# Optimization experiments

Measured on AMD Instinct MI355X. Metric: run time of the kernel, lower is better.

Reference implementation:

```python
import jax, jax.numpy as jnp
import numpy as np


def _conv(x, w, b, stride, pad):
    y = jax.lax.conv_general_dilated(
        x, w, (stride, stride), [(pad, pad), (pad, pad)],
        dimension_numbers=('NCHW', 'OIHW', 'NCHW'))
    return y + b[None, :, None, None]


def _maxpool(x):
    # kernel 3, stride 2, padding 1 (torch MaxPool2d semantics)
    return jax.lax.reduce_window(
        x, -jnp.inf, jax.lax.max,
        (1, 1, 3, 3), (1, 1, 2, 2), [(0, 0), (0, 0), (1, 1), (1, 1)])


def _squash(s, eps=1e-8):
    n2 = jnp.sum(s * s, axis=-1, keepdims=True)
    return s * (n2 / (1.0 + n2)) / jnp.sqrt(n2 + eps)


def setup_inputs() -> dict:
    key = jax.random.key(0)
    ks = jax.random.split(key, 17)
    s = 0.05
    inp = {
        'x': jax.random.normal(ks[0], (128, 3, 32, 32), jnp.float32),
        'cw1': jax.random.normal(ks[1], (96, 3, 3, 3), jnp.float32) * s,
        'cb1': jnp.zeros((96,), jnp.float32),
        'cw2': jax.random.normal(ks[2], (256, 96, 3, 3), jnp.float32) * s,
        'cb2': jnp.zeros((256,), jnp.float32),
        'cw3': jax.random.normal(ks[3], (384, 256, 3, 3), jnp.float32) * s,
        'cb3': jnp.zeros((384,), jnp.float32),
        'pw': jax.random.normal(ks[4], (256, 384, 3, 3), jnp.float32) * s,  # 32 caps * 8 dim
        'pb': jnp.zeros((256,), jnp.float32),
        'Wcaps': jax.random.normal(ks[5], (100, 1152, 16, 8), jnp.float32) * s,
        'fw1': jax.random.normal(ks[6], (1600, 4096), jnp.float32) * s,
        'fb1': jnp.zeros((4096,), jnp.float32),
        'fw2': jax.random.normal(ks[7], (4096, 4096), jnp.float32) * s,
        'fb2': jnp.zeros((4096,), jnp.float32),
        'fw3': jax.random.normal(ks[8], (4096, 100), jnp.float32) * s,
        'fb3': jnp.zeros((100,), jnp.float32),
    }
    return inp


def reference(x, cw1, cb1, cw2, cb2, cw3, cb3, pw, pb, Wcaps,
              fw1, fb1, fw2, fb2, fw3, fb3):
    ROUTINGS = 3
    # AlexNet-style conv backbone
    h = jax.nn.relu(_conv(x, cw1, cb1, 1, 1))   # [B,96,32,32]
    h = _maxpool(h)                              # [B,96,16,16]
    h = jax.nn.relu(_conv(h, cw2, cb2, 1, 1))   # [B,256,16,16]
    h = _maxpool(h)                              # [B,256,8,8]
    h = jax.nn.relu(_conv(h, cw3, cb3, 1, 1))   # [B,384,8,8]
    # PrimaryCaps: conv 384 -> 32*8, k3 s1 p0 -> [B,256,6,6]
    p = _conv(h, pw, pb, 1, 0)
    u = _squash(p.reshape(p.shape[0], -1, 8))   # [B,1152,8]
    # DenseCapsule: x_hat[b,o,i,d] = sum_e W[o,i,d,e] * u[b,i,e]
    x_hat = jnp.einsum('oide,bie->boid', Wcaps, u)  # [B,100,1152,16]
    x_hat_d = jax.lax.stop_gradient(x_hat)
    b = jnp.zeros(x_hat.shape[:3], x_hat.dtype)     # [B,100,1152]
    v = None
    for r in range(ROUTINGS):
        c = jax.nn.softmax(b, axis=1)               # couple over out caps
        if r == ROUTINGS - 1:
            v = _squash(jnp.einsum('boi,boid->bod', c, x_hat))
        else:
            v = _squash(jnp.einsum('boi,boid->bod', c, x_hat_d))
            b = b + jnp.einsum('boid,bod->boi', x_hat_d, v)
    # Flatten + FC head (dropout is identity at eval)
    f = v.reshape(v.shape[0], -1)                   # [B,1600]
    f = jax.nn.relu(f @ fw1 + fb1)
    f = jax.nn.relu(f @ fw2 + fb2)
    return f @ fw3 + fb3                            # [B,100]
```

## Files before the change

### kernel.cpp

```cpp
#include <hip/hip_runtime.h>
#include <cstddef>


typedef __attribute__((ext_vector_type(8))) short bf8_t;
typedef __attribute__((ext_vector_type(4))) float f4_t;

__device__ inline void cvt_hilo8(const float* f, unsigned* h, unsigned* l)
{
  #pragma unroll
  for (int j = 0; j < 4; ++j) {
    unsigned u0 = __float_as_uint(f[2 * j]);
    unsigned u1 = __float_as_uint(f[2 * j + 1]);
    h[j] = (u0 >> 16) | (u1 & 0xFFFF0000u);
    float r0 = f[2 * j]     - __uint_as_float(u0 & 0xFFFF0000u);
    float r1 = f[2 * j + 1] - __uint_as_float(u1 & 0xFFFF0000u);
    l[j] = (__float_as_uint(r0) >> 16) | (__float_as_uint(r1) & 0xFFFF0000u);
  }
}

__device__ inline void split1(float f, unsigned short& h, unsigned short& l)
{
  unsigned u = __float_as_uint(f);
  h = (unsigned short)(u >> 16);
  float r = f - __uint_as_float(u & 0xFFFF0000u);
  l = (unsigned short)(__float_as_uint(r) >> 16);
}

__device__ inline float bf2f(unsigned short h, unsigned short l)
{
  return __uint_as_float((unsigned)h << 16) + __uint_as_float((unsigned)l << 16);
}

__device__ inline int xcd_swz(int bid, int nwg)
{
  int xcd = bid & 7, pos = bid >> 3;
  int q = nwg >> 3, r = nwg & 7;
  return (xcd < r ? xcd * (q + 1) : r * (q + 1) + (xcd - r) * q) + pos;
}

__global__ __launch_bounds__(256) void wsplit_k(
    const float* __restrict__ w, unsigned short* __restrict__ oh,
    unsigned short* __restrict__ ol, int CO, int CI)
{
  int idx = blockIdx.x * 256 + threadIdx.x;
  int ci = idx % CI;
  int t2 = idx / CI;
  int r = t2 % 9, co = t2 / 9;
  float f = w[((size_t)co * CI + ci) * 9 + r];
  unsigned short h, l;
  split1(f, h, l);
  oh[idx] = h; ol[idx] = l;
}

__global__ __launch_bounds__(256) void conv1_k(
    const float* __restrict__ x, const float* __restrict__ wt,
    const float* __restrict__ bias, unsigned short* __restrict__ oh,
    unsigned short* __restrict__ ol)
{
  int idx = blockIdx.x * 256 + threadIdx.x;
  int w = idx & 31, h = (idx >> 5) & 31, b = idx >> 10;
  int co0 = blockIdx.y * 24;

  float xv[27];
  const float* xb = x + (size_t)b * 3072;
  #pragma unroll
  for (int ci = 0; ci < 3; ++ci)
    #pragma unroll
    for (int dh = 0; dh < 3; ++dh) {
      int ih = h + dh - 1;
      #pragma unroll
      for (int dw = 0; dw < 3; ++dw) {
        int iw = w + dw - 1;
        bool ok = ((unsigned)ih < 32u) & ((unsigned)iw < 32u);
        xv[ci * 9 + dh * 3 + dw] = ok ? xb[(ci << 10) + (ih << 5) + iw] : 0.f;
      }
    }

  size_t obase = ((size_t)b * 1024 + (h << 5) + w) * 96 + co0;
  const float* wp = wt + (size_t)co0 * 27;
  #pragma unroll 2
  for (int cp = 0; cp < 12; ++cp) {
    float a0 = bias[co0 + 2 * cp], a1 = bias[co0 + 2 * cp + 1];
    #pragma unroll
    for (int k = 0; k < 27; ++k) {
      a0 += xv[k] * wp[(2 * cp) * 27 + k];
      a1 += xv[k] * wp[(2 * cp + 1) * 27 + k];
    }
    a0 = fmaxf(a0, 0.f); a1 = fmaxf(a1, 0.f);
    unsigned short h0, l0, h1, l1;
    split1(a0, h0, l0); split1(a1, h1, l1);
    *(unsigned*)(oh + obase + 2 * cp) = (unsigned)h0 | ((unsigned)h1 << 16);
    *(unsigned*)(ol + obase + 2 * cp) = (unsigned)l0 | ((unsigned)l1 << 16);
  }
}

template <int C, int H>
__global__ __launch_bounds__(256) void maxpool_bf(
    const unsigned short* __restrict__ inh, const unsigned short* __restrict__ inl,
    unsigned short* __restrict__ outh, unsigned short* __restrict__ outl)
{
  constexpr int Ho = H >> 1;
  int idx = blockIdx.x * 256 + threadIdx.x;
  int c = idx % C;
  int q = idx / C;
  int wo = q % Ho;
  int q2 = q / Ho;
  int ho = q2 % Ho, b = q2 / Ho;
  float best = -3.4e38f;
  unsigned short bh = 0, bl = 0;
  #pragma unroll
  for (int dh = 0; dh < 3; ++dh) {
    int ih = 2 * ho - 1 + dh;
    if ((unsigned)ih >= (unsigned)H) continue;
    #pragma unroll
    for (int dw = 0; dw < 3; ++dw) {
      int iw = 2 * wo - 1 + dw;
      if ((unsigned)iw >= (unsigned)H) continue;
      size_t off = ((size_t)(b * H + ih) * H + iw) * C + c;
      unsigned short uh = inh[off], ul = inl[off];
      float f = bf2f(uh, ul);
      if (f > best) { best = f; bh = uh; bl = ul; }
    }
  }
  outh[idx] = bh; outl[idx] = bl;
}

__global__ __launch_bounds__(256) void bias_split_k(
    const float* __restrict__ in, const float* __restrict__ bias,
    unsigned short* __restrict__ oh, unsigned short* __restrict__ ol,
    int C, int total2, int nz, size_t plane)
{
  int idx = blockIdx.x * 256 + threadIdx.x;
  if (idx >= total2) return;
  int e0 = idx * 2;
  int c = e0 % C;
  float f0 = 0.f, f1 = 0.f;
  for (int z = 0; z < nz; ++z) {
    f0 += in[z * plane + e0];
    f1 += in[z * plane + e0 + 1];
  }
  f0 = fmaxf(f0 + bias[c], 0.f);
  f1 = fmaxf(f1 + bias[c + 1], 0.f);
  unsigned short h0, l0, h1, l1;
  split1(f0, h0, l0); split1(f1, h1, l1);
  *(unsigned*)(oh + e0) = (unsigned)h0 | ((unsigned)h1 << 16);
  *(unsigned*)(ol + e0) = (unsigned)l0 | ((unsigned)l1 << 16);
}

__global__ __launch_bounds__(256) void bias_reduce_k(
    const float* __restrict__ in, const float* __restrict__ bias,
    float* __restrict__ out, int N, int total, int relu, int nz, size_t plane)
{
  int idx = blockIdx.x * 256 + threadIdx.x;
  if (idx >= total) return;
  float vv = 0.f;
  for (int z = 0; z < nz; ++z) vv += in[z * plane + idx];
  vv += bias[idx % N];
  if (relu) vv = fmaxf(vv, 0.f);
  out[idx] = vv;
}

template <int CI, int H, int PAD, int WO, int CO, int MT, bool SPLIT>
__device__ __forceinline__ void conv_core(
    const unsigned short* __restrict__ inh, const unsigned short* __restrict__ inl,
    const unsigned short* __restrict__ wh, const unsigned short* __restrict__ wl,
    const float* __restrict__ bias, unsigned short* __restrict__ outh,
    unsigned short* __restrict__ outl, float* __restrict__ outf,
    int relu, int KC, size_t plane)
{
  constexpr int K = CI * 9;
  constexpr int NPIX = WO * WO;
  __shared__ uint4 LDS[2560];
  uint4* Ah = LDS;
  uint4* Al = LDS + 640;
  uint4* Bh = LDS + 1280;
  uint4* Bl = LDS + 1920;

  int id = xcd_swz(blockIdx.x, gridDim.x);
  int ntile = id / MT, mtile = id - ntile * MT;
  int n0 = ntile * 128, m0 = mtile * 128;
  int kbeg = SPLIT ? blockIdx.z * KC : 0;
  int kend = SPLIT ? kbeg + KC : K;
  float* outz = SPLIT ? outf + (size_t)blockIdx.z * plane : outf;

  int t = threadIdx.x;
  int lane = t & 63;
  int wave = __builtin_amdgcn_readfirstlane(t >> 6);
  int wm = wave & 1, wn = wave >> 1;
  int lr = lane & 15, lq = lane >> 4;

  int srow = (t >> 2) & 63;
  int kc8 = (t & 3) * 8;
  int sidx = srow * 5 + (t & 3);

  int ih0g[2], iw0g[2];
  size_t ibaseg[2];
  #pragma unroll
  for (int g = 0; g < 2; ++g) {
    int pix = m0 + g * 64 + srow;
    int bpix = pix / NPIX, xy = pix - bpix * NPIX;
    int ho = xy / WO, wo = xy - ho * WO;
    ih0g[g] = ho - PAD; iw0g[g] = wo - PAD;
    ibaseg[g] = (size_t)bpix * H * H;
  }

  uint4 pah[2], pal_[2], pbh[2], pbl[2];
  auto loadA = [&](int k0) {
    int r = k0 / CI;
    int cib = k0 - r * CI + kc8;
    int dh = r / 3, dw = r - dh * 3;
    #pragma unroll
    for (int g = 0; g < 2; ++g) {
      int ih = ih0g[g] + dh, iw = iw0g[g] + dw;
      bool ok = ((unsigned)ih < (unsigned)H) & ((unsigned)iw < (unsigned)H);
      if (ok) {
        size_t ad = (ibaseg[g] + (size_t)ih * H + iw) * CI + cib;
        pah[g] = *(const uint4*)(inh + ad);
        pal_[g] = *(const uint4*)(inl + ad);
      } else {
        pah[g] = make_uint4(0u, 0u, 0u, 0u);
        pal_[g] = make_uint4(0u, 0u, 0u, 0u);
      }
    }
  };
  auto loadB = [&](int k0) {
    #pragma unroll
    for (int g = 0; g < 2; ++g) {
      size_t ad = (size_t)(n0 + g * 64 + srow) * K + k0 + kc8;
      pbh[g] = *(const uint4*)(wh + ad);
      pbl[g] = *(const uint4*)(wl + ad);
    }
  };

  loadA(kbeg); loadB(kbeg);
  f4_t acc[4][4];
  #pragma unroll
  for (int mt = 0; mt < 4; ++mt)
    #pragma unroll
    for (int nt = 0; nt < 4; ++nt) acc[mt][nt] = (f4_t)0.0f;

  for (int k0 = kbeg; k0 < kend; k0 += 32) {
    if (k0 > kbeg) __syncthreads();
    Ah[sidx] = pah[0]; Ah[320 + sidx] = pah[1];
    Al[sidx] = pal_[0]; Al[320 + sidx] = pal_[1];
    Bh[sidx] = pbh[0]; Bh[320 + sidx] = pbh[1];
    Bl[sidx] = pbl[0]; Bl[320 + sidx] = pbl[1];
    __syncthreads();
    if (k0 + 32 < kend) { loadA(k0 + 32); loadB(k0 + 32); }

    int aBase = wm * 320 + lr * 5 + lq;
    int bBase = wn * 320 + lr * 5 + lq;
    bf8_t bvh[4], bvl[4];
    #pragma unroll
    for (int nt = 0; nt < 4; ++nt) {
      bvh[nt] = *(const bf8_t*)&Bh[bBase + nt * 80];
      bvl[nt] = *(const bf8_t*)&Bl[bBase + nt * 80];
    }
    #pragma unroll
    for (int mt = 0; mt < 4; ++mt) {
      bf8_t avh = *(const bf8_t*)&Ah[aBase + mt * 80];
      bf8_t avl = *(const bf8_t*)&Al[aBase + mt * 80];
      #pragma unroll
      for (int nt = 0; nt < 4; ++nt) {
        acc[mt][nt] = __builtin_amdgcn_mfma_f32_16x16x32_bf16(avh, bvh[nt], acc[mt][nt], 0, 0, 0);
        acc[mt][nt] = __builtin_amdgcn_mfma_f32_16x16x32_bf16(avh, bvl[nt], acc[mt][nt], 0, 0, 0);
        acc[mt][nt] = __builtin_amdgcn_mfma_f32_16x16x32_bf16(avl, bvh[nt], acc[mt][nt], 0, 0, 0);
      }
    }
  }

  if (SPLIT) {
    #pragma unroll
    for (int mt = 0; mt < 4; ++mt)
      #pragma unroll
      for (int nt = 0; nt < 4; ++nt)
        #pragma unroll
        for (int r = 0; r < 4; ++r) {
          int m = m0 + wm * 64 + mt * 16 + lq * 4 + r;
          int n = n0 + wn * 64 + nt * 16 + lr;
          outz[(size_t)m * CO + n] = acc[mt][nt][r];
        }
  } else {
    float* scratch = (float*)LDS;
    for (int ph = 0; ph < 2; ++ph) {
      __syncthreads();
      if (wm == ph) {
        #pragma unroll
        for (int mt = 0; mt < 4; ++mt)
          #pragma unroll
          for (int nt = 0; nt < 4; ++nt)
            #pragma unroll
            for (int r = 0; r < 4; ++r)
              scratch[(mt * 16 + lq * 4 + r) * 128 + wn * 64 + nt * 16 + lr] =
                  acc[mt][nt][r];
      }
      __syncthreads();
      #pragma unroll
      for (int s = 0; s < 4; ++s) {
        int task = t + s * 256;
        int row = task >> 4;
        int c8 = (task & 15) * 8;
        const float* sr = &scratch[row * 128 + c8];
        float4 f0 = *(const float4*)sr;
        float4 f1 = *(const float4*)(sr + 4);
        float f[8] = {f0.x, f0.y, f0.z, f0.w, f1.x, f1.y, f1.z, f1.w};
        unsigned hh[4], ll[4];
        #pragma unroll
        for (int j = 0; j < 4; ++j) {
          float v0 = f[2 * j]     + bias[n0 + c8 + 2 * j];
          float v1 = f[2 * j + 1] + bias[n0 + c8 + 2 * j + 1];
          if (relu) { v0 = fmaxf(v0, 0.f); v1 = fmaxf(v1, 0.f); }
          unsigned short h0, l0, h1, l1;
          split1(v0, h0, l0); split1(v1, h1, l1);
          hh[j] = (unsigned)h0 | ((unsigned)h1 << 16);
          ll[j] = (unsigned)l0 | ((unsigned)l1 << 16);
        }
        size_t ad = (size_t)(m0 + ph * 64 + row) * CO + n0 + c8;
        *(uint4*)(outh + ad) = make_uint4(hh[0], hh[1], hh[2], hh[3]);
        *(uint4*)(outl + ad) = make_uint4(ll[0], ll[1], ll[2], ll[3]);
      }
    }
  }
}

__global__ __launch_bounds__(256) void conv2gemm(
    const unsigned short* __restrict__ inh, const unsigned short* __restrict__ inl,
    const unsigned short* __restrict__ wh, const unsigned short* __restrict__ wl,
    const float* __restrict__ bias, unsigned short* __restrict__ outh,
    unsigned short* __restrict__ outl)
{
  conv_core<96, 16, 1, 16, 256, 256, false>(inh, inl, wh, wl, bias, outh, outl,
                                            nullptr, 1, 0, 0);
}

__global__ __launch_bounds__(256) void conv3gemm(
    const unsigned short* __restrict__ inh, const unsigned short* __restrict__ inl,
    const unsigned short* __restrict__ wh, const unsigned short* __restrict__ wl,
    float* __restrict__ outf)
{
  conv_core<256, 8, 1, 8, 384, 64, true>(inh, inl, wh, wl, nullptr, nullptr,
                                         nullptr, outf, 0, 768, 3145728);
}

__global__ __launch_bounds__(256) void pcapsgemm(
    const unsigned short* __restrict__ inh, const unsigned short* __restrict__ inl,
    const unsigned short* __restrict__ wh, const unsigned short* __restrict__ wl,
    float* __restrict__ outf)
{
  conv_core<384, 8, 0, 6, 256, 36, true>(inh, inl, wh, wl, nullptr, nullptr,
                                         nullptr, outf, 0, 576, 1179648);
}

__global__ __launch_bounds__(256) void fc_mfma(
    const float* __restrict__ A, const float* __restrict__ W,
    float* __restrict__ C, int K, int N, int KC, size_t plane)
{
  __shared__ uint4 Ah[256], Al[256], Bh[256], Bl[256];
  int n0 = blockIdx.x * 64, m0 = blockIdx.y * 64;
  int kbeg = blockIdx.z * KC, kend = kbeg + KC;
  float* Cz = C + (size_t)blockIdx.z * plane;
  int t = threadIdx.x;
  int lane = t & 63;
  int wave = __builtin_amdgcn_readfirstlane(t >> 6);
  int wm = wave & 1, wn = wave >> 1;
  int lr = lane & 15, lq = lane >> 4;
  int smA = t >> 2, sgA = t & 3;

  float fa[8], fb[8];
  auto loadA = [&](int k0) {
    const float4* ap = (const float4*)(A + (size_t)(m0 + smA) * K + k0 + sgA * 8);
    float4 a0 = ap[0], a1 = ap[1];
    fa[0] = a0.x; fa[1] = a0.y; fa[2] = a0.z; fa[3] = a0.w;
    fa[4] = a1.x; fa[5] = a1.y; fa[6] = a1.z; fa[7] = a1.w;
  };
  auto loadB = [&](int k0) {
    const float* wp = W + (size_t)(k0 + wave * 8) * N + n0 + lane;
    #pragma unroll
    for (int j = 0; j < 8; ++j) fb[j] = wp[(size_t)j * N];
  };

  loadA(kbeg); loadB(kbeg);
  f4_t acc[2][2];
  #pragma unroll
  for (int mt = 0; mt < 2; ++mt)
    #pragma unroll
    for (int nt = 0; nt < 2; ++nt) acc[mt][nt] = (f4_t)0.0f;

  for (int k0 = kbeg; k0 < kend; k0 += 32) {
    if (k0 > kbeg) __syncthreads();
    unsigned ha[4], la[4], hb[4], lb[4];
    cvt_hilo8(fa, ha, la);
    cvt_hilo8(fb, hb, lb);
    Ah[sgA * 64 + smA] = make_uint4(ha[0], ha[1], ha[2], ha[3]);
    Al[sgA * 64 + smA] = make_uint4(la[0], la[1], la[2], la[3]);
    Bh[wave * 64 + lane] = make_uint4(hb[0], hb[1], hb[2], hb[3]);
    Bl[wave * 64 + lane] = make_uint4(lb[0], lb[1], lb[2], lb[3]);
    __syncthreads();
    if (k0 + 32 < kend) { loadA(k0 + 32); loadB(k0 + 32); }
    bf8_t av_h[2], av_l[2], bv_h[2], bv_l[2];
    #pragma unroll
    for (int mt = 0; mt < 2; ++mt) {
      int ui = lq * 64 + wm * 32 + mt * 16 + lr;
      av_h[mt] = *(const bf8_t*)&Ah[ui];
      av_l[mt] = *(const bf8_t*)&Al[ui];
    }
    #pragma unroll
    for (int nt = 0; nt < 2; ++nt) {
      int ui = lq * 64 + wn * 32 + nt * 16 + lr;
      bv_h[nt] = *(const bf8_t*)&Bh[ui];
      bv_l[nt] = *(const bf8_t*)&Bl[ui];
    }
    #pragma unroll
    for (int mt = 0; mt < 2; ++mt)
      #pragma unroll
      for (int nt = 0; nt < 2; ++nt) {
        acc[mt][nt] = __builtin_amdgcn_mfma_f32_16x16x32_bf16(av_h[mt], bv_h[nt], acc[mt][nt], 0, 0, 0);
        acc[mt][nt] = __builtin_amdgcn_mfma_f32_16x16x32_bf16(av_h[mt], bv_l[nt], acc[mt][nt], 0, 0, 0);
        acc[mt][nt] = __builtin_amdgcn_mfma_f32_16x16x32_bf16(av_l[mt], bv_h[nt], acc[mt][nt], 0, 0, 0);
      }
  }
  #pragma unroll
  for (int mt = 0; mt < 2; ++mt)
    #pragma unroll
    for (int nt = 0; nt < 2; ++nt) {
      #pragma unroll
      for (int r = 0; r < 4; ++r) {
        int m = m0 + wm * 32 + mt * 16 + lq * 4 + r;
        int n = n0 + wn * 32 + nt * 16 + lr;
        Cz[(size_t)m * N + n] = acc[mt][nt][r];
      }
    }
}

__global__ __launch_bounds__(256) void squash8_k(
    const float* __restrict__ p, const float* __restrict__ pb,
    float* __restrict__ ut)
{
  int idx = blockIdx.x * 256 + threadIdx.x;
  if (idx >= 147456) return;
  int b = idx & 127, i = idx >> 7;
  float pv[8];
  #pragma unroll
  for (int e = 0; e < 8; ++e) {
    int f = i * 8 + e;
    int co = f / 36, pix = f - co * 36;
    size_t base = ((size_t)b * 36 + pix) * 256 + co;
    float s = 0.f;
    #pragma unroll
    for (int z = 0; z < 6; ++z) s += p[(size_t)z * 1179648 + base];
    pv[e] = s + pb[co];
  }
  float n2 = 0.f;
  #pragma unroll
  for (int e = 0; e < 8; ++e) n2 += pv[e] * pv[e];
  float sc = (n2 / (1.f + n2)) * rsqrtf(n2 + 1e-8f);
  #pragma unroll
  for (int e = 0; e < 8; ++e)
    ut[(size_t)i * 1024 + e * 128 + b] = pv[e] * sc;
}

__global__ __launch_bounds__(256) void caps_squash16(
    const float* __restrict__ s, float* __restrict__ v, float* __restrict__ vt)
{
  int idx = blockIdx.x * 256 + threadIdx.x;
  if (idx >= 12800) return;
  int b = idx / 100, o = idx % 100;
  float vv[16];
  #pragma unroll
  for (int d = 0; d < 16; ++d) vv[d] = 0.f;
  #pragma unroll
  for (int z = 0; z < 8; ++z) {
    const float4* sp = (const float4*)(s + (size_t)z * 204800 + (size_t)idx * 16);
    float4 a = sp[0], bb = sp[1], c = sp[2], d4 = sp[3];
    vv[0] += a.x;  vv[1] += a.y;  vv[2] += a.z;  vv[3] += a.w;
    vv[4] += bb.x; vv[5] += bb.y; vv[6] += bb.z; vv[7] += bb.w;
    vv[8] += c.x;  vv[9] += c.y;  vv[10] += c.z; vv[11] += c.w;
    vv[12] += d4.x; vv[13] += d4.y; vv[14] += d4.z; vv[15] += d4.w;
  }
  float n2 = 0.f;
  #pragma unroll
  for (int d = 0; d < 16; ++d) n2 += vv[d] * vv[d];
  float sc = (n2 / (1.f + n2)) * rsqrtf(n2 + 1e-8f);
  float4* vp = (float4*)(v + (size_t)idx * 16);
  float4 o0 = {vv[0] * sc, vv[1] * sc, vv[2] * sc, vv[3] * sc};
  float4 o1 = {vv[4] * sc, vv[5] * sc, vv[6] * sc, vv[7] * sc};
  float4 o2 = {vv[8] * sc, vv[9] * sc, vv[10] * sc, vv[11] * sc};
  float4 o3 = {vv[12] * sc, vv[13] * sc, vv[14] * sc, vv[15] * sc};
  vp[0] = o0; vp[1] = o1; vp[2] = o2; vp[3] = o3;
  #pragma unroll
  for (int dd = 0; dd < 16; ++dd)
    vt[((size_t)o * 16 + dd) * 128 + b] = vv[dd] * sc;
}

__global__ __launch_bounds__(256) void caps_spass_mfma(
    const float* __restrict__ W, const float* __restrict__ ut,
    const float* __restrict__ ct, float* __restrict__ s, int uniform)
{
  __shared__ uint4 Ah[512], Al[512];
  int o = blockIdx.x, ks = blockIdx.y;
  int t = threadIdx.x;
  int lane = t & 63;
  int wave = __builtin_amdgcn_readfirstlane(t >> 6);
  int lr = lane & 15, lq = lane >> 4;
  int b = t & 127, half = t >> 7;
  int i0 = ks * 144;
  float* sz = s + (size_t)ks * 204800;

  float fu[16], fc[2], fw[8];
  auto loadUC = [&](int j) {
    int ib = i0 + j * 4 + half * 2;
    #pragma unroll
    for (int q = 0; q < 2; ++q) {
      int i = ib + q;
      #pragma unroll
      for (int e = 0; e < 8; ++e)
        fu[q * 8 + e] = ut[(size_t)i * 1024 + e * 128 + b];
      fc[q] = uniform ? 0.01f : ct[((size_t)o * 1152 + i) * 128 + b];
    }
  };
  auto loadW = [&](int j) {
    int i = i0 + j * 4 + lq;
    const float4* wp = (const float4*)(W + (((size_t)o * 1152 + i) * 16 + lr) * 8);
    float4 w0 = wp[0], w1 = wp[1];
    fw[0] = w0.x; fw[1] = w0.y; fw[2] = w0.z; fw[3] = w0.w;
    fw[4] = w1.x; fw[5] = w1.y; fw[6] = w1.z; fw[7] = w1.w;
  };

  loadUC(0); loadW(0);
  f4_t acc[2];
  acc[0] = (f4_t)0.0f; acc[1] = (f4_t)0.0f;

  for (int j = 0; j < 36; ++j) {
    float cu[16];
    #pragma unroll
    for (int q = 0; q < 2; ++q)
      #pragma unroll
      for (int e = 0; e < 8; ++e)
        cu[q * 8 + e] = fc[q] * fu[q * 8 + e];
    unsigned h0[4], l0[4], h1[4], l1[4], wh[4], wl[4];
    cvt_hilo8(cu, h0, l0);
    cvt_hilo8(cu + 8, h1, l1);
    cvt_hilo8(fw, wh, wl);
    uint4 uwh = make_uint4(wh[0], wh[1], wh[2], wh[3]);
    uint4 uwl = make_uint4(wl[0], wl[1], wl[2], wl[3]);
    bf8_t bfh = *(const bf8_t*)&uwh;
    bf8_t bfl = *(const bf8_t*)&uwl;
    if (j > 0) __syncthreads();
    Ah[(half * 2 + 0) * 128 + b] = make_uint4(h0[0], h0[1], h0[2], h0[3]);
    Al[(half * 2 + 0) * 128 + b] = make_uint4(l0[0], l0[1], l0[2], l0[3]);
    Ah[(half * 2 + 1) * 128 + b] = make_uint4(h1[0], h1[1], h1[2], h1[3]);
    Al[(half * 2 + 1) * 128 + b] = make_uint4(l1[0], l1[1], l1[2], l1[3]);
    __syncthreads();
    if (j + 1 < 36) { loadUC(j + 1); loadW(j + 1); }
    #pragma unroll
    for (int mt = 0; mt < 2; ++mt) {
      int bidx = wave * 16 + mt * 64 + lr;
      bf8_t avh = *(const bf8_t*)&Ah[lq * 128 + bidx];
      bf8_t avl = *(const bf8_t*)&Al[lq * 128 + bidx];
      acc[mt] = __builtin_amdgcn_mfma_f32_16x16x32_bf16(avh, bfh, acc[mt], 0, 0, 0);
      acc[mt] = __builtin_amdgcn_mfma_f32_16x16x32_bf16(avh, bfl, acc[mt], 0, 0, 0);
      acc[mt] = __builtin_amdgcn_mfma_f32_16x16x32_bf16(avl, bfh, acc[mt], 0, 0, 0);
    }
  }
  #pragma unroll
  for (int mt = 0; mt < 2; ++mt)
    #pragma unroll
    for (int r = 0; r < 4; ++r) {
      int bb = wave * 16 + mt * 64 + lq * 4 + r;
      sz[((size_t)bb * 100 + o) * 16 + lr] = acc[mt][r];
    }
}

__global__ __launch_bounds__(256) void caps_bupdate(
    const float* __restrict__ W, const float* __restrict__ ut,
    const float* __restrict__ vt, float* __restrict__ blogt, int accum)
{
  __shared__ __align__(16) float Wt[64 * 160];
  int o = blockIdx.x, ic = blockIdx.y;
  int t = threadIdx.x;
  int lane = t & 63;
  int wave = __builtin_amdgcn_readfirstlane(t >> 6);
  int lr = lane & 15, lq = lane >> 4;
  int dhalf = (lq & 1) << 3;
  int hl = lq >> 1;

  {
    const float4* Wg = (const float4*)(W + ((size_t)o * 1152 + (size_t)ic * 64) * 128);
    for (int l = t; l < 2048; l += 256) {
      float4 w = Wg[l];
      int li = l >> 5;
      int rem = l & 31;
      int d = rem >> 1;
      int e0 = (rem & 1) << 2;
      float* dst = &Wt[li * 160 + e0 * 20 + d];
      dst[0] = w.x; dst[20] = w.y; dst[40] = w.z; dst[60] = w.w;
    }
  }

  bf8_t B1[8], B2[8];
  #pragma unroll
  for (int nt = 0; nt < 8; ++nt) {
    int b = nt * 16 + lr;
    float vv[8];
    #pragma unroll
    for (int j = 0; j < 8; ++j)
      vv[j] = vt[((size_t)o * 16 + dhalf + j) * 128 + b];
    unsigned h[4], l2[4];
    cvt_hilo8(vv, h, l2);
    uint4 uh = make_uint4(h[0], h[1], h[2], h[3]);
    uint4 ul = (lq < 2) ? make_uint4(l2[0], l2[1], l2[2], l2[3])
                        : make_uint4(0u, 0u, 0u, 0u);
    B1[nt] = *(const bf8_t*)&uh;
    B2[nt] = *(const bf8_t*)&ul;
  }
  __syncthreads();

  unsigned lomask = hl ? 0xFFFF0000u : 0u;

  for (int mi = 0; mi < 8; ++mi) {
    int mt = wave * 8 + mi;
    int liA = mt * 2 + (lr >> 3);
    int eA = lr & 7;
    const float* wp = &Wt[liA * 160 + eA * 20 + dhalf];
    float4 wa = *(const float4*)wp;
    float4 wb = *(const float4*)(wp + 4);
    float fw[8] = {wa.x, wa.y, wa.z, wa.w, wb.x, wb.y, wb.z, wb.w};
    unsigned ha[4];
    #pragma unroll
    for (int j = 0; j < 4; ++j) {
      float f0 = fw[2 * j], f1 = fw[2 * j + 1];
      f0 -= __uint_as_float(__float_as_uint(f0) & lomask);
      f1 -= __uint_as_float(__float_as_uint(f1) & lomask);
      ha[j] = (__float_as_uint(f0) >> 16) | (__float_as_uint(f1) & 0xFFFF0000u);
    }
    uint4 ua = make_uint4(ha[0], ha[1], ha[2], ha[3]);
    bf8_t A = *(const bf8_t*)&ua;

    int gi = ic * 64 + mt * 2 + hl;
    const float* up = ut + (size_t)gi * 1024 + (size_t)(((lq & 1) << 2)) * 128;
    #pragma unroll
    for (int nt = 0; nt < 8; ++nt) {
      f4_t acc = (f4_t)0.0f;
      acc = __builtin_amdgcn_mfma_f32_16x16x32_bf16(A, B1[nt], acc, 0, 0, 0);
      acc = __builtin_amdgcn_mfma_f32_16x16x32_bf16(A, B2[nt], acc, 0, 0, 0);
      int b = nt * 16 + lr;
      float p = acc[0] * up[b] + acc[1] * up[128 + b] +
                acc[2] * up[256 + b] + acc[3] * up[384 + b];
      p += __shfl_xor(p, 16);
      if (!(lq & 1)) {
        size_t off = ((size_t)o * 1152 + gi) * 128 + b;
        if (accum) blogt[off] += p; else blogt[off] = p;
      }
    }
  }
}

__global__ __launch_bounds__(256) void caps_softmax(
    const float* __restrict__ blogt, float* __restrict__ ct)
{
  int idx = blockIdx.x * 256 + threadIdx.x;
  if (idx >= 147456) return;
  const float* bp = blogt + idx;
  float m = -3.4e38f;
  for (int o = 0; o < 100; ++o) m = fmaxf(m, bp[(size_t)o * 147456]);
  float sum = 0.f;
  for (int o = 0; o < 100; ++o) sum += __expf(bp[(size_t)o * 147456] - m);
  float inv = 1.f / sum;
  for (int o = 0; o < 100; ++o)
    ct[(size_t)o * 147456 + idx] = __expf(bp[(size_t)o * 147456] - m) * inv;
}

__global__ __launch_bounds__(128) void fc3_seed(
    const float* __restrict__ bias, float* __restrict__ out)
{
  int idx = blockIdx.x * 128 + threadIdx.x;
  if (idx < 12800) out[idx] = bias[idx % 100];
}

__global__ __launch_bounds__(128) void fc3_sk(
    const float* __restrict__ A, const float* __restrict__ W,
    float* __restrict__ out)
{
  __shared__ float Al[1024];
  int m = blockIdx.x, z = blockIdx.y, t = threadIdx.x;
  int kbeg = z * 1024;
  const float* ap = A + (size_t)m * 4096 + kbeg;
  for (int l = t; l < 1024; l += 128) Al[l] = ap[l];
  __syncthreads();
  if (t < 100) {
    float acc = 0.f;
    const float* wp = W + (size_t)kbeg * 100 + t;
    #pragma unroll 8
    for (int k = 0; k < 1024; ++k) acc += Al[k] * wp[(size_t)k * 100];
    atomicAdd(out + m * 100 + t, acc);
  }
}

extern "C" void kernel_launch(void* const* d_in, const int* in_sizes, int n_in,
                              void* d_out, int out_size, void* d_ws, size_t ws_size,
                              hipStream_t stream)
{
  (void)in_sizes; (void)n_in; (void)out_size; (void)ws_size;
  const float* x   = (const float*)d_in[0];
  const float* cw1 = (const float*)d_in[1];
  const float* cb1 = (const float*)d_in[2];
  const float* cw2 = (const float*)d_in[3];
  const float* cb2 = (const float*)d_in[4];
  const float* cw3 = (const float*)d_in[5];
  const float* cb3 = (const float*)d_in[6];
  const float* pw  = (const float*)d_in[7];
  const float* pb  = (const float*)d_in[8];
  const float* Wc  = (const float*)d_in[9];
  const float* fw1 = (const float*)d_in[10];
  const float* fb1 = (const float*)d_in[11];
  const float* fw2 = (const float*)d_in[12];
  const float* fb2 = (const float*)d_in[13];
  const float* fw3 = (const float*)d_in[14];
  const float* fb3 = (const float*)d_in[15];
  float* ws = (float*)d_ws;

  const size_t OFF_A  = 0;
  const size_t OFF_B  = 12582912;
  const size_t OFF_U  = 15728640;
  const size_t OFF_P  = 16908288;
  const size_t OFF_C  = 18087936;
  const size_t OFF_V  = 32833536;
  const size_t OFF_F1 = 33243136;
  const size_t OFF_F2 = 33767424;

  float* ut    = ws + OFF_U;
  float* vt    = ws + OFF_P;
  float* ct    = ws + OFF_C;
  float* v     = ws + OFF_V;
  float* sz    = ws + OFF_B;
  float* f1    = ws + OFF_F1;
  float* f2    = ws + OFF_F2;
  float* blogt = ws + OFF_A;
  float* fcz   = ws + OFF_C;

  unsigned short* h1h  = (unsigned short*)(ws + OFF_A);
  unsigned short* h1l  = h1h + 12582912;
  unsigned short* mp1h = (unsigned short*)(ws + OFF_B);
  unsigned short* mp1l = mp1h + 3145728;
  unsigned short* h2h  = (unsigned short*)(ws + OFF_A);
  unsigned short* h2l  = h2h + 8388608;
  unsigned short* mp2h = (unsigned short*)(ws + OFF_B);
  unsigned short* mp2l = mp2h + 2097152;
  unsigned short* h3h  = (unsigned short*)(ws + OFF_A);
  unsigned short* h3l  = h3h + 3145728;

  unsigned short* wc2h = (unsigned short*)(ws + OFF_C);
  unsigned short* wc2l = wc2h + 221184;
  unsigned short* wc3h = wc2l + 221184;
  unsigned short* wc3l = wc3h + 884736;
  unsigned short* pwth = wc3l + 884736;
  unsigned short* pwtl = pwth + 884736;
  float* zscr = ws + OFF_C + 2097152;

  wsplit_k<<<864, 256, 0, stream>>>(cw2, wc2h, wc2l, 256, 96);
  wsplit_k<<<3456, 256, 0, stream>>>(cw3, wc3h, wc3l, 384, 256);
  wsplit_k<<<3456, 256, 0, stream>>>(pw,  pwth, pwtl, 256, 384);

  conv1_k<<<dim3(512, 4), 256, 0, stream>>>(x, cw1, cb1, h1h, h1l);
  maxpool_bf<96, 32><<<12288, 256, 0, stream>>>(h1h, h1l, mp1h, mp1l);
  conv2gemm<<<512, 256, 0, stream>>>(mp1h, mp1l, wc2h, wc2l, cb2, h2h, h2l);
  maxpool_bf<256, 16><<<8192, 256, 0, stream>>>(h2h, h2l, mp2h, mp2l);
  conv3gemm<<<dim3(192, 1, 3), 256, 0, stream>>>(mp2h, mp2l, wc3h, wc3l, zscr);
  bias_split_k<<<6144, 256, 0, stream>>>(zscr, cb3, h3h, h3l, 384, 1572864, 3, 3145728);
  pcapsgemm<<<dim3(72, 1, 6), 256, 0, stream>>>(h3h, h3l, pwth, pwtl, zscr);
  squash8_k<<<576, 256, 0, stream>>>(zscr, pb, ut);

  for (int r = 0; r < 3; ++r) {
    if (r == 0) {
      caps_spass_mfma<<<dim3(100, 8), 256, 0, stream>>>(Wc, ut, ut , sz, 1);
    } else {
      caps_softmax<<<576, 256, 0, stream>>>(blogt, ct);
      caps_spass_mfma<<<dim3(100, 8), 256, 0, stream>>>(Wc, ut, ct, sz, 0);
    }
    caps_squash16<<<50, 256, 0, stream>>>(sz, v, vt);
    if (r < 2)
      caps_bupdate<<<dim3(100, 18), 256, 0, stream>>>(Wc, ut, vt, blogt, r);
  }

  fc_mfma<<<dim3(64, 2, 2), 256, 0, stream>>>(v,  fw1, fcz, 1600, 4096, 800, 524288);
  bias_reduce_k<<<2048, 256, 0, stream>>>(fcz, fb1, f1, 4096, 524288, 1, 2, 524288);
  fc_mfma<<<dim3(64, 2, 4), 256, 0, stream>>>(f1, fw2, fcz, 4096, 4096, 1024, 524288);
  bias_reduce_k<<<2048, 256, 0, stream>>>(fcz, fb2, f2, 4096, 524288, 1, 4, 524288);
  fc3_seed<<<100, 128, 0, stream>>>(fb3, (float*)d_out);
  fc3_sk<<<dim3(128, 4), 128, 0, stream>>>(f2, fw3, (float*)d_out);
}
```

Before: 1.155 ms.

## Swizzle conv GEMM LDS tiles, stage split-K output via LDS, raise conv3 splits

Replaces the padded LDS layout (stride 5 uint4 per row) with an XOR-swizzled layout (stride 4). This shrinks LDS use while still aiming to avoid bank conflicts on the MFMA operand reads. The split-K epilogue now goes through the LDS scratch tile (padded to 132), so its global stores become coalesced float4 writes instead of scattered scalar stores. Conv3 split-K goes from 3 to 4 chunks for more parallelism, at the cost of an extra partial plane for the bias reduction to read and write.

```diff
diff --git a/kernel.cpp b/kernel.cpp
--- a/kernel.cpp
+++ b/kernel.cpp
@@ -170,11 +170,11 @@
 {
   constexpr int K = CI * 9;
   constexpr int NPIX = WO * WO;
-  __shared__ uint4 LDS[2560];
-  uint4* Ah = LDS;
-  uint4* Al = LDS + 640;
-  uint4* Bh = LDS + 1280;
-  uint4* Bl = LDS + 1920;
+  __shared__ __align__(16) float LDSF[8448];
+  uint4* Ah = (uint4*)LDSF;
+  uint4* Al = Ah + 512;
+  uint4* Bh = Ah + 1024;
+  uint4* Bl = Ah + 1536;
 
   int id = xcd_swz(blockIdx.x, gridDim.x);
   int ntile = id / MT, mtile = id - ntile * MT;
@@ -191,7 +191,7 @@
 
   int srow = (t >> 2) & 63;
   int kc8 = (t & 3) * 8;
-  int sidx = srow * 5 + (t & 3);
+  int sidx = srow * 4 + ((t & 3) ^ (srow & 3));
 
   int ih0g[2], iw0g[2];
   size_t ibaseg[2];
@@ -241,25 +241,26 @@
 
   for (int k0 = kbeg; k0 < kend; k0 += 32) {
     if (k0 > kbeg) __syncthreads();
-    Ah[sidx] = pah[0]; Ah[320 + sidx] = pah[1];
-    Al[sidx] = pal_[0]; Al[320 + sidx] = pal_[1];
-    Bh[sidx] = pbh[0]; Bh[320 + sidx] = pbh[1];
-    Bl[sidx] = pbl[0]; Bl[320 + sidx] = pbl[1];
+    Ah[sidx] = pah[0]; Ah[256 + sidx] = pah[1];
+    Al[sidx] = pal_[0]; Al[256 + sidx] = pal_[1];
+    Bh[sidx] = pbh[0]; Bh[256 + sidx] = pbh[1];
+    Bl[sidx] = pbl[0]; Bl[256 + sidx] = pbl[1];
     __syncthreads();
     if (k0 + 32 < kend) { loadA(k0 + 32); loadB(k0 + 32); }
 
-    int aBase = wm * 320 + lr * 5 + lq;
-    int bBase = wn * 320 + lr * 5 + lq;
+    int xk = lq ^ (lr & 3);
+    int aBase = wm * 256 + lr * 4 + xk;
+    int bBase = wn * 256 + lr * 4 + xk;
     bf8_t bvh[4], bvl[4];
     #pragma unroll
     for (int nt = 0; nt < 4; ++nt) {
-      bvh[nt] = *(const bf8_t*)&Bh[bBase + nt * 80];
-      bvl[nt] = *(const bf8_t*)&Bl[bBase + nt * 80];
+      bvh[nt] = *(const bf8_t*)&Bh[bBase + nt * 64];
+      bvl[nt] = *(const bf8_t*)&Bl[bBase + nt * 64];
     }
     #pragma unroll
     for (int mt = 0; mt < 4; ++mt) {
-      bf8_t avh = *(const bf8_t*)&Ah[aBase + mt * 80];
-      bf8_t avl = *(const bf8_t*)&Al[aBase + mt * 80];
+      bf8_t avh = *(const bf8_t*)&Ah[aBase + mt * 64];
+      bf8_t avl = *(const bf8_t*)&Al[aBase + mt * 64];
       #pragma unroll
       for (int nt = 0; nt < 4; ++nt) {
         acc[mt][nt] = __builtin_amdgcn_mfma_f32_16x16x32_bf16(avh, bvh[nt], acc[mt][nt], 0, 0, 0);
@@ -269,38 +270,36 @@
     }
   }
 
-  if (SPLIT) {
-    #pragma unroll
-    for (int mt = 0; mt < 4; ++mt)
-      #pragma unroll
-      for (int nt = 0; nt < 4; ++nt)
+  float* scratch = LDSF;
+  for (int ph = 0; ph < 2; ++ph) {
+    __syncthreads();
+    if (wm == ph) {
+      #pragma unroll
+      for (int mt = 0; mt < 4; ++mt)
         #pragma unroll
-        for (int r = 0; r < 4; ++r) {
-          int m = m0 + wm * 64 + mt * 16 + lq * 4 + r;
-          int n = n0 + wn * 64 + nt * 16 + lr;
-          outz[(size_t)m * CO + n] = acc[mt][nt][r];
-        }
-  } else {
-    float* scratch = (float*)LDS;
-    for (int ph = 0; ph < 2; ++ph) {
-      __syncthreads();
-      if (wm == ph) {
-        #pragma unroll
-        for (int mt = 0; mt < 4; ++mt)
+        for (int nt = 0; nt < 4; ++nt)
           #pragma unroll
-          for (int nt = 0; nt < 4; ++nt)
-            #pragma unroll
-            for (int r = 0; r < 4; ++r)
-              scratch[(mt * 16 + lq * 4 + r) * 128 + wn * 64 + nt * 16 + lr] =
-                  acc[mt][nt][r];
+          for (int r = 0; r < 4; ++r)
+            scratch[(mt * 16 + lq * 4 + r) * 132 + wn * 64 + nt * 16 + lr] =
+                acc[mt][nt][r];
+    }
+    __syncthreads();
+    if (SPLIT) {
+      #pragma unroll
+      for (int s = 0; s < 8; ++s) {
+        int idx = t + s * 256;
+        int row = idx >> 5;
+        int c4 = idx & 31;
+        float4 f = *(const float4*)&scratch[row * 132 + c4 * 4];
+        *(float4*)(outz + (size_t)(m0 + ph * 64 + row) * CO + n0 + c4 * 4) = f;
       }
-      __syncthreads();
+    } else {
       #pragma unroll
       for (int s = 0; s < 4; ++s) {
         int task = t + s * 256;
         int row = task >> 4;
         int c8 = (task & 15) * 8;
-        const float* sr = &scratch[row * 128 + c8];
+        const float* sr = &scratch[row * 132 + c8];
         float4 f0 = *(const float4*)sr;
         float4 f1 = *(const float4*)(sr + 4);
         float f[8] = {f0.x, f0.y, f0.z, f0.w, f1.x, f1.y, f1.z, f1.w};
@@ -339,7 +338,7 @@
     float* __restrict__ outf)
 {
   conv_core<256, 8, 1, 8, 384, 64, true>(inh, inl, wh, wl, nullptr, nullptr,
-                                         nullptr, outf, 0, 768, 3145728);
+                                         nullptr, outf, 0, 576, 3145728);
 }
 
 __global__ __launch_bounds__(256) void pcapsgemm(
@@ -765,8 +764,8 @@
   maxpool_bf<96, 32><<<12288, 256, 0, stream>>>(h1h, h1l, mp1h, mp1l);
   conv2gemm<<<512, 256, 0, stream>>>(mp1h, mp1l, wc2h, wc2l, cb2, h2h, h2l);
   maxpool_bf<256, 16><<<8192, 256, 0, stream>>>(h2h, h2l, mp2h, mp2l);
-  conv3gemm<<<dim3(192, 1, 3), 256, 0, stream>>>(mp2h, mp2l, wc3h, wc3l, zscr);
-  bias_split_k<<<6144, 256, 0, stream>>>(zscr, cb3, h3h, h3l, 384, 1572864, 3, 3145728);
+  conv3gemm<<<dim3(192, 1, 4), 256, 0, stream>>>(mp2h, mp2l, wc3h, wc3l, zscr);
+  bias_split_k<<<6144, 256, 0, stream>>>(zscr, cb3, h3h, h3l, 384, 1572864, 4, 3145728);
   pcapsgemm<<<dim3(72, 1, 6), 256, 0, stream>>>(h3h, h3l, pwth, pwtl, zscr);
   squash8_k<<<576, 256, 0, stream>>>(zscr, pb, ut);
 
```

Measured after the change: 1.140 ms. No clear change (-1.4%).
